# Performance work log

Measured on AMD Instinct MI355X. Metric: run time of the kernel, lower is better.

## Reference

```python
import jax, jax.numpy as jnp
import numpy as np

O = 100000   # num objects
R = 1000000  # num triplets
D = 128      # per-slot feature dim (input_dim[0]=input_dim[1]=input_dim[2])
SUM_D = 3 * D  # MLP in/out width
H = 256      # hidden_dim


def setup_inputs() -> dict:
    key = jax.random.key(0)
    k1, k2, k3, k4, k5 = jax.random.split(key, 5)
    object_feats = jax.random.normal(k1, (O, D), dtype=jnp.float32)
    relation_feats = jax.random.normal(k2, (R, D), dtype=jnp.float32)
    triplet = jax.random.randint(k3, (R, 3), 0, O, dtype=jnp.int64)
    # MLP: Linear(SUM_D->H) + ReLU + Linear(H->SUM_D), kaiming-normal init
    W1 = jax.random.normal(k4, (SUM_D, H), dtype=jnp.float32) * np.sqrt(2.0 / SUM_D)
    b1 = jnp.zeros((H,), dtype=jnp.float32)
    W2 = jax.random.normal(k5, (H, SUM_D), dtype=jnp.float32) * np.sqrt(2.0 / H)
    b2 = jnp.zeros((SUM_D,), dtype=jnp.float32)
    return {
        "object_feats": object_feats,
        "relation_feats": relation_feats,
        "W1": W1, "b1": b1, "W2": W2, "b2": b2,
        "triplet": triplet,
        "triplet_len": R,
    }


def reference(object_feats, relation_feats, W1, b1, W2, b2, triplet, triplet_len):
    t = triplet[:triplet_len]                      # [R, 3]
    subs = t[:, 0]                                 # [R]
    objs = t[:, 1]                                 # [R]
    # gather subj/obj feats, concat with relation feats -> [R, 3D]
    gcn_feat = jnp.concatenate(
        [object_feats[subs], relation_feats, object_feats[objs]], axis=1)
    # 2-layer MLP
    h = jax.nn.relu(gcn_feat @ W1 + b1)            # [R, H]
    out = h @ W2 + b2                              # [R, 3D]
    sub_out = out[:, :D]
    rel_out = out[:, D:-D]
    obj_out = out[:, -D:]
    # scatter-add back to object nodes, then mean by degree, plus residual
    acc = jnp.zeros_like(object_feats)
    acc = acc.at[subs].add(sub_out).at[objs].add(obj_out)   # [O, D]
    one = jnp.ones((triplet_len,), dtype=object_feats.dtype)
    cnt = jnp.zeros((object_feats.shape[0],), dtype=object_feats.dtype)
    cnt = cnt.at[subs].add(one).at[objs].add(one)           # [O]
    output_feat = acc / jnp.clip(cnt, 1.0)[:, None] + object_feats
    return (output_feat, rel_out, triplet, triplet_len)
```

## Files before the change

### kernel.cpp

```cpp
#include <hip/hip_runtime.h>

#define O_N 100000
#define R_N 1000000
#define DIM 128
#define SD 384
#define HD 256
#define BR 64

typedef __attribute__((ext_vector_type(8))) short short8;
typedef __attribute__((ext_vector_type(4))) float f32x4;

static __device__ __forceinline__ unsigned short f2bf(float x) {
    union { float f; unsigned int u; } v; v.f = x;
    unsigned int r = v.u + 0x7FFFu + ((v.u >> 16) & 1u);
    return (unsigned short)(r >> 16);
}

__global__ void prep_weights(const float* __restrict__ W1, const float* __restrict__ W2,
                             unsigned short* __restrict__ W1T, unsigned short* __restrict__ W2T) {
    int i = blockIdx.x * 256 + threadIdx.x;
    if (i < SD * HD) {
        int h = i / SD, k = i - h * SD;
        W1T[i] = f2bf(W1[k * HD + h]);
    } else {
        int j = i - SD * HD;
        int c = j / HD, k = j - c * HD;
        W2T[j] = f2bf(W2[k * SD + c]);
    }
}

__global__ void trip_cnt(const int* __restrict__ trip, float* __restrict__ tripOut,
                         float* __restrict__ lenOut, float* __restrict__ cnt,
                         const int* __restrict__ tlen) {
    int i = blockIdx.x * 256 + threadIdx.x;
    if (i < R_N) {
        int s = trip[3 * i], o = trip[3 * i + 1], t2 = trip[3 * i + 2];
        tripOut[3 * i]     = (float)s;
        tripOut[3 * i + 1] = (float)o;
        tripOut[3 * i + 2] = (float)t2;
        atomicAdd(&cnt[min(max(s, 0), O_N - 1)], 1.0f);
        atomicAdd(&cnt[min(max(o, 0), O_N - 1)], 1.0f);
        if (i == 0) lenOut[0] = (float)tlen[0];
    }
}

__global__ __launch_bounds__(256, 3)
void mlp_kernel(const float* __restrict__ objF, const float* __restrict__ relF,
                const unsigned short* __restrict__ W1T, const unsigned short* __restrict__ W2T,
                const float* __restrict__ b1, const float* __restrict__ b2,
                const int* __restrict__ trip,
                float* __restrict__ accB, float* __restrict__ relOut) {
    __shared__ __align__(16) unsigned char smem[49664];
    unsigned char* Xs = smem;
    unsigned char* Hs = smem;
    int* idxBuf = (int*)(smem + 49152);

    const int tid  = threadIdx.x;
    const int lane = tid & 63;
    const int w    = tid >> 6;
    const int r0   = blockIdx.x * BR;
    const int l15  = lane & 15;
    const int l4   = lane >> 4;

    if (tid < 2 * BR) {
        int rr = r0 + (tid & 63);
        int which = tid >> 6;
        idxBuf[tid] = min(max(trip[3 * rr + which], 0), O_N - 1);
    }
    __syncthreads();

    #pragma unroll
    for (int it = 0; it < 24; ++it) {
        int idx = it * 256 + tid;
        int row = idx / 96;
        int c4  = idx - row * 96;
        const float* src;
        if (c4 < 32)      src = objF + (size_t)idxBuf[row] * DIM + c4 * 4;
        else if (c4 < 64) src = relF + (size_t)(r0 + row) * DIM + (c4 - 32) * 4;
        else              src = objF + (size_t)idxBuf[BR + row] * DIM + (c4 - 64) * 4;
        f32x4 v = *(const f32x4*)src;
        unsigned long long pk =  (unsigned long long)f2bf(v.x)
                              | ((unsigned long long)f2bf(v.y) << 16)
                              | ((unsigned long long)f2bf(v.z) << 32)
                              | ((unsigned long long)f2bf(v.w) << 48);
        int byteoff = row * 768 + ((((c4 >> 1) ^ (row & 15)) << 4) + (c4 & 1) * 8);
        *(unsigned long long*)(Xs + byteoff) = pk;
    }
    __syncthreads();

    const int hW = w * 64;
    f32x4 acc1[4][4];
    #pragma unroll
    for (int a = 0; a < 4; ++a)
        #pragma unroll
        for (int b = 0; b < 4; ++b) acc1[a][b] = (f32x4)0.0f;

    #pragma unroll
    for (int ks = 0; ks < 12; ++ks) {
        int k0 = ks * 32;
        short8 af[4], bfr[4];
        #pragma unroll
        for (int mh = 0; mh < 4; ++mh) {
            int h = hW + mh * 16 + l15;
            af[mh] = *(const short8*)(W1T + h * SD + k0 + 8 * l4);
        }
        #pragma unroll
        for (int nr = 0; nr < 4; ++nr) {
            int rel = nr * 16 + l15;
            int kb  = (k0 >> 3) + l4;
            bfr[nr] = *(const short8*)(Xs + rel * 768 + ((kb ^ (rel & 15)) << 4));
        }
        #pragma unroll
        for (int mh = 0; mh < 4; ++mh)
            #pragma unroll
            for (int nr = 0; nr < 4; ++nr)
                acc1[mh][nr] = __builtin_amdgcn_mfma_f32_16x16x32_bf16(
                    af[mh], bfr[nr], acc1[mh][nr], 0, 0, 0);
    }
    __syncthreads();

    #pragma unroll
    for (int mh = 0; mh < 4; ++mh) {
        int hbase = hW + mh * 16 + 4 * l4;
        float bb0 = b1[hbase], bb1 = b1[hbase + 1], bb2 = b1[hbase + 2], bb3 = b1[hbase + 3];
        int hb   = hbase >> 3;
        int half = (hbase >> 2) & 1;
        #pragma unroll
        for (int nr = 0; nr < 4; ++nr) {
            int rel = nr * 16 + l15;
            unsigned long long pk =
                  (unsigned long long)f2bf(fmaxf(acc1[mh][nr][0] + bb0, 0.f))
                | ((unsigned long long)f2bf(fmaxf(acc1[mh][nr][1] + bb1, 0.f)) << 16)
                | ((unsigned long long)f2bf(fmaxf(acc1[mh][nr][2] + bb2, 0.f)) << 32)
                | ((unsigned long long)f2bf(fmaxf(acc1[mh][nr][3] + bb3, 0.f)) << 48);
            *(unsigned long long*)(Hs + rel * 512 + ((hb ^ (rel & 15)) << 4) + half * 8) = pk;
        }
    }
    __syncthreads();

    const int cW = w * 96;
    f32x4 acc2[4][6];
    #pragma unroll
    for (int a = 0; a < 4; ++a)
        #pragma unroll
        for (int b = 0; b < 6; ++b) acc2[a][b] = (f32x4)0.0f;

    #pragma unroll
    for (int ks = 0; ks < 8; ++ks) {
        int k0 = ks * 32;
        short8 ha[4], wb[6];
        #pragma unroll
        for (int ma = 0; ma < 4; ++ma) {
            int rel = ma * 16 + l15;
            int hb  = (k0 >> 3) + l4;
            ha[ma] = *(const short8*)(Hs + rel * 512 + ((hb ^ (rel & 15)) << 4));
        }
        #pragma unroll
        for (int nb = 0; nb < 6; ++nb) {
            int c = cW + nb * 16 + l15;
            wb[nb] = *(const short8*)(W2T + c * HD + k0 + 8 * l4);
        }
        #pragma unroll
        for (int ma = 0; ma < 4; ++ma)
            #pragma unroll
            for (int nb = 0; nb < 6; ++nb)
                acc2[ma][nb] = __builtin_amdgcn_mfma_f32_16x16x32_bf16(
                    ha[ma], wb[nb], acc2[ma][nb], 0, 0, 0);
    }

    #pragma unroll
    for (int ma = 0; ma < 4; ++ma) {
        int rloc = ma * 16 + 4 * l4;
        int rg   = r0 + rloc;
        int subs[4], objs[4];
        #pragma unroll
        for (int q = 0; q < 4; ++q) {
            subs[q] = idxBuf[rloc + q];
            objs[q] = idxBuf[BR + rloc + q];
        }
        #pragma unroll
        for (int nb = 0; nb < 6; ++nb) {
            int c = cW + nb * 16 + l15;
            float b2v = b2[c];
            #pragma unroll
            for (int q = 0; q < 4; ++q) {
                float v = acc2[ma][nb][q] + b2v;
                if (c < DIM) {
                    atomicAdd(accB + (size_t)subs[q] * DIM + c, v);
                } else if (c < 2 * DIM) {
                    relOut[(size_t)(rg + q) * DIM + (c - DIM)] = v;
                } else {
                    atomicAdd(accB + (size_t)objs[q] * DIM + (c - 2 * DIM), v);
                }
            }
        }
    }
}

__global__ void finalize(const float* __restrict__ accB, const float* __restrict__ cnt,
                         const float* __restrict__ objF, float* __restrict__ outF) {
    int i = blockIdx.x * 256 + threadIdx.x;
    if (i < O_N * DIM / 4) {
        int row = i >> 5;
        float c = fmaxf(cnt[row], 1.0f);
        f32x4 a = ((const f32x4*)accB)[i];
        f32x4 o = ((const f32x4*)objF)[i];
        f32x4 r;
        r.x = a.x / c + o.x;
        r.y = a.y / c + o.y;
        r.z = a.z / c + o.z;
        r.w = a.w / c + o.w;
        ((f32x4*)outF)[i] = r;
    }
}

extern "C" void kernel_launch(void* const* d_in, const int* in_sizes, int n_in,
                              void* d_out, int out_size, void* d_ws, size_t ws_size,
                              hipStream_t stream) {
    const float* objF = (const float*)d_in[0];
    const float* relF = (const float*)d_in[1];
    const float* W1   = (const float*)d_in[2];
    const float* b1   = (const float*)d_in[3];
    const float* W2   = (const float*)d_in[4];
    const float* b2   = (const float*)d_in[5];
    const int*   trip = (const int*)d_in[6];
    const int*   tlen = (const int*)d_in[7];

    float* outF    = (float*)d_out;
    float* relOut  = outF + (size_t)O_N * DIM;
    float* tripOut = relOut + (size_t)R_N * DIM;
    float* lenOut  = tripOut + (size_t)R_N * 3;

    unsigned short* W1T = (unsigned short*)d_ws;
    unsigned short* W2T = W1T + SD * HD;
    float* accB = (float*)(W2T + SD * HD);
    float* cnt  = accB + (size_t)O_N * DIM;

    hipMemsetAsync(accB, 0, ((size_t)O_N * DIM + O_N) * sizeof(float), stream);
    prep_weights<<<(2 * SD * HD) / 256, 256, 0, stream>>>(W1, W2, W1T, W2T);
    trip_cnt<<<(R_N + 255) / 256, 256, 0, stream>>>(trip, tripOut, lenOut, cnt, tlen);
    mlp_kernel<<<R_N / BR, 256, 0, stream>>>(objF, relF, W1T, W2T, b1, b2, trip, accB, relOut);
    finalize<<<(O_N * DIM / 4 + 255) / 256, 256, 0, stream>>>(accB, cnt, objF, outF);
}
```

Measured before the change: 1.634 ms.

## Pre-convert features to bf16 and stage MLP inputs via direct global-to-LDS loads

Adds a separate pass that converts object and relation features to bf16 buffers in workspace. The MLP kernel then gathers these bf16 rows straight into shared memory with global_load_lds, using a swizzled source mapping so the XOR layout is kept without a register round trip. This halves the bytes gathered per triplet and removes the per-element conversion from the main kernel. The cost is an extra full read of the relation features plus a bf16 write, on the order of 0.75 GB of extra traffic.

Result: faster. 1.519 ms (-7.1%).

```diff
diff --git a/kernel.cpp b/kernel.cpp
--- a/kernel.cpp
+++ b/kernel.cpp
@@ -6,6 +6,8 @@
 #define SD 384
 #define HD 256
 #define BR 64
+#define OBJ8 (O_N * DIM / 8)
+#define REL8 (R_N * DIM / 8)
 
 typedef __attribute__((ext_vector_type(8))) short short8;
 typedef __attribute__((ext_vector_type(4))) float f32x4;
@@ -14,6 +16,12 @@
     union { float f; unsigned int u; } v; v.f = x;
     unsigned int r = v.u + 0x7FFFu + ((v.u >> 16) & 1u);
     return (unsigned short)(r >> 16);
+}
+static __device__ __forceinline__ unsigned long long pack4(f32x4 v) {
+    return  (unsigned long long)f2bf(v.x)
+         | ((unsigned long long)f2bf(v.y) << 16)
+         | ((unsigned long long)f2bf(v.z) << 32)
+         | ((unsigned long long)f2bf(v.w) << 48);
 }
 
 __global__ void prep_weights(const float* __restrict__ W1, const float* __restrict__ W2,
@@ -27,6 +35,20 @@
         int c = j / HD, k = j - c * HD;
         W2T[j] = f2bf(W2[k * SD + c]);
     }
+}
+
+__global__ void conv_bf16(const float* __restrict__ objF, const float* __restrict__ relF,
+                          unsigned short* __restrict__ objBF, unsigned short* __restrict__ relBF) {
+    long long i = (long long)blockIdx.x * 256 + threadIdx.x;
+    if (i >= (long long)OBJ8 + REL8) return;
+    const float* s; unsigned short* d;
+    if (i < OBJ8) { s = objF + i * 8;           d = objBF + i * 8; }
+    else          { long long j = i - OBJ8; s = relF + j * 8; d = relBF + j * 8; }
+    f32x4 v0 = ((const f32x4*)s)[0];
+    f32x4 v1 = ((const f32x4*)s)[1];
+    unsigned long long* dd = (unsigned long long*)d;
+    dd[0] = pack4(v0);
+    dd[1] = pack4(v1);
 }
 
 __global__ void trip_cnt(const int* __restrict__ trip, float* __restrict__ tripOut,
@@ -45,7 +67,7 @@
 }
 
 __global__ __launch_bounds__(256, 3)
-void mlp_kernel(const float* __restrict__ objF, const float* __restrict__ relF,
+void mlp_kernel(const unsigned short* __restrict__ objBF, const unsigned short* __restrict__ relBF,
                 const unsigned short* __restrict__ W1T, const unsigned short* __restrict__ W2T,
                 const float* __restrict__ b1, const float* __restrict__ b2,
                 const int* __restrict__ trip,
@@ -63,28 +85,27 @@
     const int l4   = lane >> 4;
 
     if (tid < 2 * BR) {
-        int rr = r0 + (tid & 63);
+        int rr = r0 + (tid & (BR - 1));
         int which = tid >> 6;
         idxBuf[tid] = min(max(trip[3 * rr + which], 0), O_N - 1);
     }
     __syncthreads();
 
     #pragma unroll
-    for (int it = 0; it < 24; ++it) {
-        int idx = it * 256 + tid;
-        int row = idx / 96;
-        int c4  = idx - row * 96;
-        const float* src;
-        if (c4 < 32)      src = objF + (size_t)idxBuf[row] * DIM + c4 * 4;
-        else if (c4 < 64) src = relF + (size_t)(r0 + row) * DIM + (c4 - 32) * 4;
-        else              src = objF + (size_t)idxBuf[BR + row] * DIM + (c4 - 64) * 4;
-        f32x4 v = *(const f32x4*)src;
-        unsigned long long pk =  (unsigned long long)f2bf(v.x)
-                              | ((unsigned long long)f2bf(v.y) << 16)
-                              | ((unsigned long long)f2bf(v.z) << 32)
-                              | ((unsigned long long)f2bf(v.w) << 48);
-        int byteoff = row * 768 + ((((c4 >> 1) ^ (row & 15)) << 4) + (c4 & 1) * 8);
-        *(unsigned long long*)(Xs + byteoff) = pk;
+    for (int j = 0; j < 12; ++j) {
+        int seg = w * 12 + j;
+        int a   = seg * 64 + lane;
+        int row = a / 48;
+        int p   = a - row * 48;
+        int u   = p ^ (row & 15);
+        const unsigned short* src;
+        if (u < 16)      src = objBF + (size_t)idxBuf[row] * DIM + u * 8;
+        else if (u < 32) src = relBF + (size_t)(r0 + row) * DIM + (u - 16) * 8;
+        else             src = objBF + (size_t)idxBuf[BR + row] * DIM + (u - 32) * 8;
+        __builtin_amdgcn_global_load_lds(
+            (const __attribute__((address_space(1))) void*)src,
+            (__attribute__((address_space(3))) void*)(Xs + seg * 1024),
+            16, 0, 0);
     }
     __syncthreads();
 
@@ -235,10 +256,13 @@
     unsigned short* W2T = W1T + SD * HD;
     float* accB = (float*)(W2T + SD * HD);
     float* cnt  = accB + (size_t)O_N * DIM;
-
-    hipMemsetAsync(accB, 0, ((size_t)O_N * DIM + O_N) * sizeof(float), stream);
+    unsigned short* objBF = (unsigned short*)(cnt + O_N);
+    unsigned short* relBF = objBF + (size_t)O_N * DIM;
+
+    (void)hipMemsetAsync(accB, 0, ((size_t)O_N * DIM + O_N) * sizeof(float), stream);
     prep_weights<<<(2 * SD * HD) / 256, 256, 0, stream>>>(W1, W2, W1T, W2T);
+    conv_bf16<<<(OBJ8 + REL8 + 255) / 256, 256, 0, stream>>>(objF, relF, objBF, relBF);
     trip_cnt<<<(R_N + 255) / 256, 256, 0, stream>>>(trip, tripOut, lenOut, cnt, tlen);
-    mlp_kernel<<<R_N / BR, 256, 0, stream>>>(objF, relF, W1T, W2T, b1, b2, trip, accB, relOut);
+    mlp_kernel<<<R_N / BR, 256, 0, stream>>>(objBF, relBF, W1T, W2T, b1, b2, trip, accB, relOut);
     finalize<<<(O_N * DIM / 4 + 255) / 256, 256, 0, stream>>>(accB, cnt, objF, outF);
 }
```

## Pre-convert object feats to bf16 and load GEMM1 operands directly from global

Applied to the files above, without the earlier changes.

Adds a kernel that converts object features to bf16 once, so the MLP kernel gathers half the bytes per subject and object row. GEMM1 now loads its B fragments directly from global memory (bf16 objects, fp32 relations converted in registers) instead of staging the concatenated input in LDS. This removes a staging pass and a barrier and cuts LDS use from about 49KB to 32KB, with launch_bounds dropped. In exchange, fragment loads are scattered, so each wave issues many small gathers that may be less coalesced, and one extra pass over the object table is added.

After: 2.788 ms. 70.6% more time.

```diff
diff --git a/kernel.cpp b/kernel.cpp
--- a/kernel.cpp
+++ b/kernel.cpp
@@ -6,6 +6,8 @@
 #define SD 384
 #define HD 256
 #define BR 64
+#define NT (R_N / BR)
+#define OBJ8 (O_N * DIM / 8)
 
 typedef __attribute__((ext_vector_type(8))) short short8;
 typedef __attribute__((ext_vector_type(4))) float f32x4;
@@ -14,6 +16,12 @@
     union { float f; unsigned int u; } v; v.f = x;
     unsigned int r = v.u + 0x7FFFu + ((v.u >> 16) & 1u);
     return (unsigned short)(r >> 16);
+}
+static __device__ __forceinline__ unsigned long long pack4(f32x4 v) {
+    return  (unsigned long long)f2bf(v.x)
+         | ((unsigned long long)f2bf(v.y) << 16)
+         | ((unsigned long long)f2bf(v.z) << 32)
+         | ((unsigned long long)f2bf(v.w) << 48);
 }
 
 __global__ void prep_weights(const float* __restrict__ W1, const float* __restrict__ W2,
@@ -26,6 +34,17 @@
         int j = i - SD * HD;
         int c = j / HD, k = j - c * HD;
         W2T[j] = f2bf(W2[k * SD + c]);
+    }
+}
+
+__global__ void conv_obj(const float* __restrict__ objF, unsigned short* __restrict__ objBF) {
+    int i = blockIdx.x * 256 + threadIdx.x;
+    if (i < OBJ8) {
+        f32x4 v0 = ((const f32x4*)(objF + (size_t)i * 8))[0];
+        f32x4 v1 = ((const f32x4*)(objF + (size_t)i * 8))[1];
+        unsigned long long* dd = (unsigned long long*)(objBF + (size_t)i * 8);
+        dd[0] = pack4(v0);
+        dd[1] = pack4(v1);
     }
 }
 
@@ -44,16 +63,13 @@
     }
 }
 
-__global__ __launch_bounds__(256, 3)
-void mlp_kernel(const float* __restrict__ objF, const float* __restrict__ relF,
-                const unsigned short* __restrict__ W1T, const unsigned short* __restrict__ W2T,
-                const float* __restrict__ b1, const float* __restrict__ b2,
-                const int* __restrict__ trip,
-                float* __restrict__ accB, float* __restrict__ relOut) {
-    __shared__ __align__(16) unsigned char smem[49664];
-    unsigned char* Xs = smem;
-    unsigned char* Hs = smem;
-    int* idxBuf = (int*)(smem + 49152);
+__global__ void mlp_kernel(const unsigned short* __restrict__ objBF, const float* __restrict__ relF,
+                           const unsigned short* __restrict__ W1T, const unsigned short* __restrict__ W2T,
+                           const float* __restrict__ b1, const float* __restrict__ b2,
+                           const int* __restrict__ trip,
+                           float* __restrict__ accB, float* __restrict__ relOut) {
+    __shared__ __align__(16) unsigned char Hs[32768];
+    __shared__ int idxBuf[128];
 
     const int tid  = threadIdx.x;
     const int lane = tid & 63;
@@ -61,63 +77,60 @@
     const int r0   = blockIdx.x * BR;
     const int l15  = lane & 15;
     const int l4   = lane >> 4;
-
-    if (tid < 2 * BR) {
-        int rr = r0 + (tid & 63);
-        int which = tid >> 6;
-        idxBuf[tid] = min(max(trip[3 * rr + which], 0), O_N - 1);
-    }
-    __syncthreads();
-
-    #pragma unroll
-    for (int it = 0; it < 24; ++it) {
-        int idx = it * 256 + tid;
-        int row = idx / 96;
-        int c4  = idx - row * 96;
-        const float* src;
-        if (c4 < 32)      src = objF + (size_t)idxBuf[row] * DIM + c4 * 4;
-        else if (c4 < 64) src = relF + (size_t)(r0 + row) * DIM + (c4 - 32) * 4;
-        else              src = objF + (size_t)idxBuf[BR + row] * DIM + (c4 - 64) * 4;
-        f32x4 v = *(const f32x4*)src;
-        unsigned long long pk =  (unsigned long long)f2bf(v.x)
-                              | ((unsigned long long)f2bf(v.y) << 16)
-                              | ((unsigned long long)f2bf(v.z) << 32)
-                              | ((unsigned long long)f2bf(v.w) << 48);
-        int byteoff = row * 768 + ((((c4 >> 1) ^ (row & 15)) << 4) + (c4 & 1) * 8);
-        *(unsigned long long*)(Xs + byteoff) = pk;
-    }
-    __syncthreads();
-
-    const int hW = w * 64;
+    const int hW   = w * 64;
+    const int cW   = w * 96;
+
+    int subG[4], objG[4];
+    #pragma unroll
+    for (int nr = 0; nr < 4; ++nr) {
+        int rr = r0 + nr * 16 + l15;
+        subG[nr] = min(max(trip[3 * rr], 0), O_N - 1);
+        objG[nr] = min(max(trip[3 * rr + 1], 0), O_N - 1);
+    }
+
     f32x4 acc1[4][4];
     #pragma unroll
     for (int a = 0; a < 4; ++a)
         #pragma unroll
         for (int b = 0; b < 4; ++b) acc1[a][b] = (f32x4)0.0f;
 
-    #pragma unroll
-    for (int ks = 0; ks < 12; ++ks) {
-        int k0 = ks * 32;
-        short8 af[4], bfr[4];
-        #pragma unroll
-        for (int mh = 0; mh < 4; ++mh) {
-            int h = hW + mh * 16 + l15;
-            af[mh] = *(const short8*)(W1T + h * SD + k0 + 8 * l4);
-        }
-        #pragma unroll
-        for (int nr = 0; nr < 4; ++nr) {
-            int rel = nr * 16 + l15;
-            int kb  = (k0 >> 3) + l4;
-            bfr[nr] = *(const short8*)(Xs + rel * 768 + ((kb ^ (rel & 15)) << 4));
-        }
-        #pragma unroll
-        for (int mh = 0; mh < 4; ++mh)
-            #pragma unroll
-            for (int nr = 0; nr < 4; ++nr)
-                acc1[mh][nr] = __builtin_amdgcn_mfma_f32_16x16x32_bf16(
-                    af[mh], bfr[nr], acc1[mh][nr], 0, 0, 0);
-    }
-    __syncthreads();
+    #define G1STEP(K0, BFR_EXPR)                                              \
+    {                                                                         \
+        const int k0 = (K0);                                                  \
+        short8 af[4], bfr[4];                                                 \
+        _Pragma("unroll")                                                     \
+        for (int nr = 0; nr < 4; ++nr) { BFR_EXPR; }                          \
+        _Pragma("unroll")                                                     \
+        for (int mh = 0; mh < 4; ++mh)                                        \
+            af[mh] = *(const short8*)(W1T + (hW + mh * 16 + l15) * SD + k0 + 8 * l4); \
+        _Pragma("unroll")                                                     \
+        for (int mh = 0; mh < 4; ++mh)                                        \
+            _Pragma("unroll")                                                 \
+            for (int nr = 0; nr < 4; ++nr)                                    \
+                acc1[mh][nr] = __builtin_amdgcn_mfma_f32_16x16x32_bf16(       \
+                    af[mh], bfr[nr], acc1[mh][nr], 0, 0, 0);                  \
+    }
+
+    #pragma unroll
+    for (int ks = 0; ks < 4; ++ks)
+        G1STEP(ks * 32,
+            bfr[nr] = *(const short8*)(objBF + (size_t)subG[nr] * DIM + k0 + l4 * 8));
+    #pragma unroll
+    for (int ks = 4; ks < 8; ++ks)
+        G1STEP(ks * 32,
+            {
+                const float* rp = relF + (size_t)(r0 + nr * 16 + l15) * DIM + (k0 - 128) + l4 * 8;
+                f32x4 a0 = ((const f32x4*)rp)[0];
+                f32x4 a1 = ((const f32x4*)rp)[1];
+                union { unsigned long long q[2]; short8 v; } u;
+                u.q[0] = pack4(a0); u.q[1] = pack4(a1);
+                bfr[nr] = u.v;
+            });
+    #pragma unroll
+    for (int ks = 8; ks < 12; ++ks)
+        G1STEP(ks * 32,
+            bfr[nr] = *(const short8*)(objBF + (size_t)objG[nr] * DIM + (k0 - 256) + l4 * 8));
+    #undef G1STEP
 
     #pragma unroll
     for (int mh = 0; mh < 4; ++mh) {
@@ -136,9 +149,12 @@
             *(unsigned long long*)(Hs + rel * 512 + ((hb ^ (rel & 15)) << 4) + half * 8) = pk;
         }
     }
+    if (tid < 2 * BR) {
+        int rr = r0 + (tid & (BR - 1));
+        idxBuf[tid] = min(max(trip[3 * rr + (tid >> 6)], 0), O_N - 1);
+    }
     __syncthreads();
 
-    const int cW = w * 96;
     f32x4 acc2[4][6];
     #pragma unroll
     for (int a = 0; a < 4; ++a)
@@ -235,10 +251,12 @@
     unsigned short* W2T = W1T + SD * HD;
     float* accB = (float*)(W2T + SD * HD);
     float* cnt  = accB + (size_t)O_N * DIM;
-
-    hipMemsetAsync(accB, 0, ((size_t)O_N * DIM + O_N) * sizeof(float), stream);
+    unsigned short* objBF = (unsigned short*)(cnt + O_N);
+
+    (void)hipMemsetAsync(accB, 0, ((size_t)O_N * DIM + O_N) * sizeof(float), stream);
     prep_weights<<<(2 * SD * HD) / 256, 256, 0, stream>>>(W1, W2, W1T, W2T);
+    conv_obj<<<(OBJ8 + 255) / 256, 256, 0, stream>>>(objF, objBF);
     trip_cnt<<<(R_N + 255) / 256, 256, 0, stream>>>(trip, tripOut, lenOut, cnt, tlen);
-    mlp_kernel<<<R_N / BR, 256, 0, stream>>>(objF, relF, W1T, W2T, b1, b2, trip, accB, relOut);
+    mlp_kernel<<<NT, 256, 0, stream>>>(objBF, relF, W1T, W2T, b1, b2, trip, accB, relOut);
     finalize<<<(O_N * DIM / 4 + 255) / 256, 256, 0, stream>>>(accB, cnt, objF, outF);
 }
```
